# Kernel optimization log

Measured on AMD Instinct MI355X. Metric: run time of the kernel, lower is better.

The kernel has to match this reference:

```python
import jax, jax.numpy as jnp
import numpy as np

B, N_PER, SEQ, DIN, OUT = 16384, 16, 168, 16, 24
H1, H2, OUTF, NH, OLEN, DEG = 128, 128, 64, 4, 128, 4
DH = OUTF // NH
N = B * N_PER
E = N * DEG


def setup_inputs() -> dict:
    key = jax.random.key(0)
    ks = jax.random.split(key, 24)
    rng = np.random.default_rng(0)
    # DEG out-edges per node, destinations confined to the node's own graph block
    src = np.repeat(np.arange(N, dtype=np.int64), DEG)
    dst = (src // N_PER) * N_PER + rng.integers(0, N_PER, size=E).astype(np.int64)
    edge_index = jnp.stack([jnp.asarray(src), jnp.asarray(dst)])
    batch = jnp.asarray(np.arange(N, dtype=np.int64) // N_PER)
    g = lambda i, shape: jax.random.normal(ks[i], shape, jnp.float32) * 0.05
    return dict(
        x=jax.random.normal(ks[0], (N, SEQ), jnp.float32),
        y=jax.random.normal(ks[1], (N, OUT), jnp.float32),
        edge_index=edge_index, batch=batch,
        w1l=g(2, (SEQ, H1)), w1r=g(3, (SEQ, H1)), b1=jnp.zeros((H1,), jnp.float32),
        w2l=g(4, (H1, H2)), w2r=g(5, (H1, H2)), b2=jnp.zeros((H2,), jnp.float32),
        w3l=g(6, (H2, OUTF)), w3r=g(7, (H2, OUTF)), b3=jnp.zeros((OUTF,), jnp.float32),
        tcn_w=g(8, (OUTF, OUTF, 2)), tcn_b=jnp.zeros((OUTF,), jnp.float32),
        wq=g(9, (OUTF, OUTF)), wk=g(10, (OUTF, OUTF)), wv=g(11, (OUTF, OUTF)), wo=g(12, (OUTF, OUTF)),
        wproj=g(13, (OUTF, OLEN)), bproj=jnp.zeros((OLEN,), jnp.float32),
        fc1_w=g(14, (DIN, OLEN, 64)), fc1_b=jnp.zeros((DIN, 64), jnp.float32),
        fc2_w=g(15, (DIN, 64, OUT)), fc2_b=jnp.zeros((DIN, OUT), jnp.float32),
    )


def _sage(h, src, dst, wl, wr, b):
    # PyG SAGEConv: lin_l(mean-aggregated neighbors) + lin_r(self)
    agg = jax.ops.segment_sum(h[src], dst, num_segments=N)
    cnt = jax.ops.segment_sum(jnp.ones((src.shape[0],), h.dtype), dst, num_segments=N)
    agg = agg / jnp.maximum(cnt, 1.0)[:, None]
    return agg @ wl + h @ wr + b


def _forward(x, y, src, dst, w1l, w1r, b1, w2l, w2r, b2, w3l, w3r, b3,
             tcn_w, tcn_b, wq, wk, wv, wo, wproj, bproj, fc1_w, fc1_b, fc2_w, fc2_b):
    h = jax.nn.relu(_sage(x, src, dst, w1l, w1r, b1))
    h = jax.nn.relu(_sage(h, src, dst, w2l, w2r, b2))
    h = _sage(h, src, dst, w3l, w3r, b3)              # [N, 64]
    # ragged->dense batch: batch ids are block-constant with equal counts,
    # so the per-element Python stacking in the original is exactly a reshape
    xb = h.reshape(B, N_PER, OUTF)
    yb = y.reshape(B, N_PER, OUT)
    xt = xb.transpose(0, 2, 1)                        # [B, 64, n]
    # SMTA: causal TCN (kernel 2, channels [64]) with residual, dropout inert
    xp = jnp.pad(xt, ((0, 0), (0, 0), (1, 0)))
    conv = jax.lax.conv_general_dilated(xp, tcn_w, (1,), 'VALID',
                                        dimension_numbers=('NCH', 'OIH', 'NCH'))
    t = jax.nn.relu(conv + tcn_b[None, :, None]) + xt  # [B, 64, n]
    # 4-head self-attention over the node axis
    s = t.transpose(0, 2, 1)                          # [B, n, 64]
    q = (s @ wq).reshape(B, N_PER, NH, DH)
    k = (s @ wk).reshape(B, N_PER, NH, DH)
    v = (s @ wv).reshape(B, N_PER, NH, DH)
    scale = 1.0 / float(np.sqrt(DH))
    att = jax.nn.softmax(jnp.einsum('bqhd,bkhd->bhqk', q, k) * scale, axis=-1)
    o = jnp.einsum('bhqk,bkhd->bqhd', att, v).reshape(B, N_PER, OUTF) @ wo
    feat = o.mean(axis=1) @ wproj + bproj             # [B, 128]
    # per-variable fc heads, vectorized over the DIN heads
    h1 = jax.nn.relu(jnp.einsum('bf,kfh->kbh', feat, fc1_w) + fc1_b[:, None, :])
    pred = jnp.einsum('kbh,kho->kbo', h1, fc2_w) + fc2_b[:, None, :]  # [DIN, B, OUT]
    return pred, yb


def reference(x, y, edge_index, batch, w1l, w1r, b1, w2l, w2r, b2, w3l, w3r, b3,
              tcn_w, tcn_b, wq, wk, wv, wo, wproj, bproj, fc1_w, fc1_b, fc2_w, fc2_b):
    src, dst = edge_index[0], edge_index[1]
    return _forward(x, y, src, dst, w1l, w1r, b1, w2l, w2r, b2, w3l, w3r, b3,
                    tcn_w, tcn_b, wq, wk, wv, wo, wproj, bproj,
                    fc1_w, fc1_b, fc2_w, fc2_b)
```

## Files before the change

kernel.cpp:

```cpp
#include <hip/hip_runtime.h>
#include <cstdint>
#include <cstddef>


typedef __attribute__((ext_vector_type(8))) __bf16 bf16x8;
typedef __attribute__((ext_vector_type(4))) float  f32x4;

#define MFMA16(a,b,c) __builtin_amdgcn_mfma_f32_16x16x32_bf16((a),(b),(c),0,0,0)
#define FENCE() __threadfence_block()

#define NGR    16384
#define EDGES  1048576
#define PRED_ELEMS (16*16384*24)

#define O_W1L 0
#define O_W1R 24576
#define O_W2L 49152
#define O_W2R 65536
#define O_W3L 81920
#define O_W3R 90112
#define O_T0  98304
#define O_T1  102400
#define O_WQ  106496
#define O_WK  110592
#define O_WV  114688
#define O_WO  118784
#define O_FC1 122880
#define O_FC2 253952
#define O_FEAT 286720
#define PREP_TOT 286720

static __device__ __forceinline__ unsigned short f2bf(float f){
  unsigned int u = __builtin_bit_cast(unsigned int, f);
  u += 0x7FFFu + ((u >> 16) & 1u);
  return (unsigned short)(u >> 16);
}
static __device__ __forceinline__ float bf2f(unsigned short h){
  return __builtin_bit_cast(float, (unsigned int)h << 16);
}
static __device__ __forceinline__ bf16x8 ld8(const unsigned short* p){
  return __builtin_bit_cast(bf16x8, *(const uint4*)p);
}
static __device__ __forceinline__ bf16x8 zero8(){
  uint4 u = make_uint4(0u,0u,0u,0u);
  return __builtin_bit_cast(bf16x8, u);
}
static __device__ __forceinline__ unsigned int pkbf2(float a, float b){
  return (unsigned int)f2bf(a) | ((unsigned int)f2bf(b)<<16);
}
static __device__ __forceinline__ bf16x8 u4bf(unsigned int a, unsigned int b,
                                              unsigned int c, unsigned int d){
  uint4 u = make_uint4(a,b,c,d);
  return __builtin_bit_cast(bf16x8, u);
}
static __device__ __forceinline__ bf16x8 shfrag(unsigned int p0, unsigned int p1,
                                                int laneA, int laneB){
  return u4bf((unsigned int)__shfl((int)p0, laneA, 64),
              (unsigned int)__shfl((int)p1, laneA, 64),
              (unsigned int)__shfl((int)p0, laneB, 64),
              (unsigned int)__shfl((int)p1, laneB, 64));
}
static __device__ __forceinline__ bf16x8 xfrag(const float* __restrict__ xrow, int k0){
  int ks = (k0 < 168) ? k0 : 0;
  float4 f0 = *(const float4*)(xrow + ks);
  float4 f1 = *(const float4*)(xrow + ks + 4);
  return u4bf(pkbf2(f0.x,f0.y), pkbf2(f0.z,f0.w),
              pkbf2(f1.x,f1.y), pkbf2(f1.z,f1.w));
}
template<int TOT, int K, int P>
static __device__ __forceinline__ void stageW(const unsigned short* __restrict__ src,
                                              unsigned short* __restrict__ dst, int tid){
  #pragma unroll
  for (int it=0; it<TOT/2048; ++it){
    int idx = it*2048 + tid*8;
    int row = idx / K, col = idx - row*K;
    *(uint4*)(dst + row*P + col) = *(const uint4*)(src + idx);
  }
}

__global__ __launch_bounds__(256) void k_prep(
  const float* __restrict__ w1l, const float* __restrict__ w1r,
  const float* __restrict__ w2l, const float* __restrict__ w2r,
  const float* __restrict__ w3l, const float* __restrict__ w3r,
  const float* __restrict__ tcnw,
  const float* __restrict__ wq, const float* __restrict__ wk,
  const float* __restrict__ wv, const float* __restrict__ wo,
  const float* __restrict__ fc1w, const float* __restrict__ fc2w,
  unsigned short* __restrict__ W)
{
  int idx = blockIdx.x*256 + threadIdx.x;
  if (idx >= PREP_TOT) return;
  float v;
  if      (idx <  24576){ int t=idx;        int n=t/192,k=t%192; v=(k<168)? w1l[k*128+n]:0.f; }
  else if (idx <  49152){ int t=idx- 24576; int n=t/192,k=t%192; v=(k<168)? w1r[k*128+n]:0.f; }
  else if (idx <  65536){ int t=idx- 49152; int n=t/128,k=t%128; v=w2l[k*128+n]; }
  else if (idx <  81920){ int t=idx- 65536; int n=t/128,k=t%128; v=w2r[k*128+n]; }
  else if (idx <  90112){ int t=idx- 81920; int n=t/128,k=t%128; v=w3l[k*64+n]; }
  else if (idx <  98304){ int t=idx- 90112; int n=t/128,k=t%128; v=w3r[k*64+n]; }
  else if (idx < 102400){ int t=idx- 98304; int n=t/64, k=t%64;  v=tcnw[(n*64+k)*2+0]; }
  else if (idx < 106496){ int t=idx-102400; int n=t/64, k=t%64;  v=tcnw[(n*64+k)*2+1]; }
  else if (idx < 110592){ int t=idx-106496; int n=t/64, k=t%64;  v=wq[k*64+n]; }
  else if (idx < 114688){ int t=idx-110592; int n=t/64, k=t%64;  v=wk[k*64+n]; }
  else if (idx < 118784){ int t=idx-114688; int n=t/64, k=t%64;  v=wv[k*64+n]; }
  else if (idx < 122880){ int t=idx-118784; int n=t/64, k=t%64;  v=wo[k*64+n]; }
  else if (idx < 253952){ int t=idx-122880; int kh=t/8192, r=t%8192, n=r/128, k=r%128;
                          v=fc1w[kh*8192 + k*64 + n]; }
  else                  { int t=idx-253952; int kh=t/2048, r=t%2048, n=r/64,  k=r%64;
                          v=(n<24)? fc2w[kh*1536 + k*24 + n] : 0.f; }
  W[idx] = f2bf(v);
}

__global__ __launch_bounds__(256,3) void k_fused(
  const float* __restrict__ x, const int* __restrict__ edst,
  const float* __restrict__ b1, const float* __restrict__ b2,
  const float* __restrict__ b3, const float* __restrict__ tcnb,
  const float* __restrict__ wo, const float* __restrict__ wproj,
  const float* __restrict__ bproj,
  const unsigned short* __restrict__ ws0, unsigned short* __restrict__ feat)
{
  __shared__ alignas(16) unsigned char pool[4*9216];
  __shared__ alignas(16) unsigned short WB[8704];
  const int tid=threadIdx.x, w=tid>>6, lane=tid&63, quad=lane>>4, l15=lane&15;
  unsigned short* AR = (unsigned short*)(pool + w*9216);
  const int gb0 = (blockIdx.x*4 + w)*2;

  unsigned short* Hb = AR;
  unsigned short* X  = AR;
  unsigned short* T  = AR + 2304;
  unsigned short* Qb = AR;
  unsigned short* Pb = AR + 2304;
  float* OMf = (float*)AR;

  const bf16x8 Z = zero8();
  const f32x4  z = {0.f,0.f,0.f,0.f};
  const int laneA = 32*quad + l15, laneB = laneA + 16;

  bf16x8 aA[2];
  #pragma unroll
  for (int g=0; g<2; ++g){
    int dl = edst[(gb0+g)*64 + lane] & 15;
    float c4[4]; float csum = 0.f;
    #pragma unroll
    for (int ss=0; ss<4; ++ss){
      int s = quad*4 + ss; int cc = 0;
      #pragma unroll
      for (int k=0;k<4;++k) cc += (__shfl(dl, s*4+k, 64) == l15) ? 1 : 0;
      c4[ss] = (float)cc; csum += (float)cc;
    }
    csum += __shfl_xor(csum, 16, 64);
    csum += __shfl_xor(csum, 32, 64);
    float ainv = 1.f / fmaxf(csum, 1.f);
    unsigned int p0 = pkbf2(c4[0]*ainv, c4[1]*ainv);
    unsigned int p1 = pkbf2(c4[2]*ainv, c4[3]*ainv);
    bf16x8 t = shfrag(p0, p1, laneA, laneB);
    aA[g] = (quad < 2) ? t : Z;
  }

  const float* xr0 = x + (size_t)(gb0*16 + l15)*168;
  const float* xr1 = xr0 + 16*168;
  bf16x8 xa0[6], xa1[6];
  #pragma unroll
  for (int kc=0;kc<6;++kc){
    xa0[kc] = xfrag(xr0, kc*32 + quad*8);
    xa1[kc] = xfrag(xr1, kc*32 + quad*8);
  }

  #pragma unroll
  for (int cg=0; cg<4; ++cg){
    __syncthreads();
    stageW<6144,192,200>(ws0 + O_W1L + cg*6144, WB, tid);
    __syncthreads();
    f32x4 au[2][2];
    #pragma unroll
    for (int g=0;g<2;++g)
    #pragma unroll
    for (int c=0;c<2;++c) au[g][c]=z;
    #pragma unroll
    for (int kc=0;kc<6;++kc){
      #pragma unroll
      for (int c=0;c<2;++c){
        bf16x8 bl = ld8(WB + (c*16+l15)*200 + kc*32 + quad*8);
        au[0][c] = MFMA16(xa0[kc], bl, au[0][c]);
        au[1][c] = MFMA16(xa1[kc], bl, au[1][c]);
      }
    }
    bf16x8 uf[2][2];
    #pragma unroll
    for (int g=0;g<2;++g)
    #pragma unroll
    for (int c=0;c<2;++c){
      unsigned int p0 = pkbf2(au[g][c][0], au[g][c][1]);
      unsigned int p1 = pkbf2(au[g][c][2], au[g][c][3]);
      uf[g][c] = shfrag(p0,p1,laneA,laneB);
    }
    __syncthreads();
    stageW<6144,192,200>(ws0 + O_W1R + cg*6144, WB, tid);
    __syncthreads();
    f32x4 av_[2][2];
    #pragma unroll
    for (int g=0;g<2;++g)
    #pragma unroll
    for (int c=0;c<2;++c) av_[g][c]=z;
    #pragma unroll
    for (int kc=0;kc<6;++kc){
      #pragma unroll
      for (int c=0;c<2;++c){
        bf16x8 br = ld8(WB + (c*16+l15)*200 + kc*32 + quad*8);
        av_[0][c] = MFMA16(xa0[kc], br, av_[0][c]);
        av_[1][c] = MFMA16(xa1[kc], br, av_[1][c]);
      }
    }
    #pragma unroll
    for (int g=0;g<2;++g)
    #pragma unroll
    for (int c=0;c<2;++c)
      av_[g][c] = MFMA16(aA[g], uf[g][c], av_[g][c]);
    #pragma unroll
    for (int c=0;c<2;++c){
      float bb = b1[cg*32 + c*16 + l15];
      #pragma unroll
      for (int g=0;g<2;++g)
      #pragma unroll
      for (int r=0;r<4;++r)
        Hb[g*2176 + (quad*4+r)*136 + cg*32 + c*16 + l15] = f2bf(fmaxf(av_[g][c][r]+bb, 0.f));
    }
  }
  FENCE();

  {
    ushort4 os[4][2][2];
    #pragma unroll
    for (int cg=0; cg<4; ++cg){
      __syncthreads();
      stageW<4096,128,136>(ws0 + O_W2L + cg*4096, WB, tid);
      __syncthreads();
      bf16x8 uf[2][2];
      {
        f32x4 au[2][2];
        #pragma unroll
        for (int g=0;g<2;++g)
        #pragma unroll
        for (int c=0;c<2;++c) au[g][c]=z;
        #pragma unroll
        for (int kc=0;kc<4;++kc){
          bf16x8 a0 = ld8(Hb +        l15*136 + kc*32 + quad*8);
          bf16x8 a1 = ld8(Hb + 2176 + l15*136 + kc*32 + quad*8);
          #pragma unroll
          for (int c=0;c<2;++c){
            bf16x8 bl = ld8(WB + (c*16+l15)*136 + kc*32 + quad*8);
            au[0][c] = MFMA16(a0, bl, au[0][c]);
            au[1][c] = MFMA16(a1, bl, au[1][c]);
          }
        }
        #pragma unroll
        for (int g=0;g<2;++g)
        #pragma unroll
        for (int c=0;c<2;++c){
          unsigned int p0 = pkbf2(au[g][c][0], au[g][c][1]);
          unsigned int p1 = pkbf2(au[g][c][2], au[g][c][3]);
          uf[g][c] = shfrag(p0,p1,laneA,laneB);
        }
      }
      __syncthreads();
      stageW<4096,128,136>(ws0 + O_W2R + cg*4096, WB, tid);
      __syncthreads();
      {
        f32x4 av_[2][2];
        #pragma unroll
        for (int g=0;g<2;++g)
        #pragma unroll
        for (int c=0;c<2;++c) av_[g][c]=z;
        #pragma unroll
        for (int kc=0;kc<4;++kc){
          bf16x8 a0 = ld8(Hb +        l15*136 + kc*32 + quad*8);
          bf16x8 a1 = ld8(Hb + 2176 + l15*136 + kc*32 + quad*8);
          #pragma unroll
          for (int c=0;c<2;++c){
            bf16x8 br = ld8(WB + (c*16+l15)*136 + kc*32 + quad*8);
            av_[0][c] = MFMA16(a0, br, av_[0][c]);
            av_[1][c] = MFMA16(a1, br, av_[1][c]);
          }
        }
        #pragma unroll
        for (int g=0;g<2;++g)
        #pragma unroll
        for (int c=0;c<2;++c)
          av_[g][c] = MFMA16(aA[g], uf[g][c], av_[g][c]);
        #pragma unroll
        for (int c=0;c<2;++c){
          float bb = b2[cg*32 + c*16 + l15];
          #pragma unroll
          for (int g=0;g<2;++g){
            ushort4 p;
            p.x = f2bf(fmaxf(av_[g][c][0]+bb, 0.f));
            p.y = f2bf(fmaxf(av_[g][c][1]+bb, 0.f));
            p.z = f2bf(fmaxf(av_[g][c][2]+bb, 0.f));
            p.w = f2bf(fmaxf(av_[g][c][3]+bb, 0.f));
            os[cg][g][c] = p;
          }
        }
      }
    }
    #pragma unroll
    for (int cg=0; cg<4; ++cg)
    #pragma unroll
    for (int g=0; g<2; ++g)
    #pragma unroll
    for (int c=0; c<2; ++c){
      unsigned short* bp = Hb + g*2176 + cg*32 + c*16 + l15;
      ushort4 p = os[cg][g][c];
      bp[(quad*4+0)*136] = p.x;
      bp[(quad*4+1)*136] = p.y;
      bp[(quad*4+2)*136] = p.z;
      bp[(quad*4+3)*136] = p.w;
    }
  }
  FENCE();

  {
    bf16x8 uf[2][4];
    __syncthreads();
    stageW<8192,128,136>(ws0 + O_W3L, WB, tid);
    __syncthreads();
    {
      f32x4 au[2][4];
      #pragma unroll
      for (int g=0;g<2;++g)
      #pragma unroll
      for (int c=0;c<4;++c) au[g][c]=z;
      #pragma unroll
      for (int kc=0;kc<4;++kc){
        bf16x8 a0 = ld8(Hb +        l15*136 + kc*32 + quad*8);
        bf16x8 a1 = ld8(Hb + 2176 + l15*136 + kc*32 + quad*8);
        #pragma unroll
        for (int c=0;c<4;++c){
          bf16x8 bl = ld8(WB + (c*16+l15)*136 + kc*32 + quad*8);
          au[0][c] = MFMA16(a0, bl, au[0][c]);
          au[1][c] = MFMA16(a1, bl, au[1][c]);
        }
      }
      #pragma unroll
      for (int g=0;g<2;++g)
      #pragma unroll
      for (int c=0;c<4;++c){
        unsigned int p0 = pkbf2(au[g][c][0], au[g][c][1]);
        unsigned int p1 = pkbf2(au[g][c][2], au[g][c][3]);
        uf[g][c] = shfrag(p0,p1,laneA,laneB);
      }
    }
    __syncthreads();
    stageW<8192,128,136>(ws0 + O_W3R, WB, tid);
    __syncthreads();
    {
      f32x4 av_[2][4];
      #pragma unroll
      for (int g=0;g<2;++g)
      #pragma unroll
      for (int c=0;c<4;++c) av_[g][c]=z;
      #pragma unroll
      for (int kc=0;kc<4;++kc){
        bf16x8 a0 = ld8(Hb +        l15*136 + kc*32 + quad*8);
        bf16x8 a1 = ld8(Hb + 2176 + l15*136 + kc*32 + quad*8);
        #pragma unroll
        for (int c=0;c<4;++c){
          bf16x8 br = ld8(WB + (c*16+l15)*136 + kc*32 + quad*8);
          av_[0][c] = MFMA16(a0, br, av_[0][c]);
          av_[1][c] = MFMA16(a1, br, av_[1][c]);
        }
      }
      #pragma unroll
      for (int g=0;g<2;++g)
      #pragma unroll
      for (int c=0;c<4;++c)
        av_[g][c] = MFMA16(aA[g], uf[g][c], av_[g][c]);
      #pragma unroll
      for (int c=0;c<4;++c){
        float bb = b3[c*16 + l15];
        #pragma unroll
        for (int g=0;g<2;++g)
        #pragma unroll
        for (int r=0;r<4;++r)
          X[g*1152 + (quad*4+r)*72 + c*16 + l15] = f2bf(av_[g][c][r] + bb);
      }
    }
  }
  FENCE();

  {
    f32x4 acct[2][4];
    #pragma unroll
    for (int g=0;g<2;++g)
    #pragma unroll
    for (int c=0;c<4;++c) acct[g][c]=z;
    __syncthreads();
    stageW<4096,64,72>(ws0 + O_T0, WB, tid);
    __syncthreads();
    #pragma unroll
    for (int kc=0;kc<2;++kc){
      bf16x8 as0 = (l15>0) ? ld8(X +        (l15-1)*72 + kc*32 + quad*8) : Z;
      bf16x8 as1 = (l15>0) ? ld8(X + 1152 + (l15-1)*72 + kc*32 + quad*8) : Z;
      #pragma unroll
      for (int c=0;c<4;++c){
        bf16x8 w0 = ld8(WB + (c*16+l15)*72 + kc*32 + quad*8);
        acct[0][c] = MFMA16(as0, w0, acct[0][c]);
        acct[1][c] = MFMA16(as1, w0, acct[1][c]);
      }
    }
    __syncthreads();
    stageW<4096,64,72>(ws0 + O_T1, WB, tid);
    __syncthreads();
    #pragma unroll
    for (int kc=0;kc<2;++kc){
      bf16x8 ax0 = ld8(X +        l15*72 + kc*32 + quad*8);
      bf16x8 ax1 = ld8(X + 1152 + l15*72 + kc*32 + quad*8);
      #pragma unroll
      for (int c=0;c<4;++c){
        bf16x8 w1 = ld8(WB + (c*16+l15)*72 + kc*32 + quad*8);
        acct[0][c] = MFMA16(ax0, w1, acct[0][c]);
        acct[1][c] = MFMA16(ax1, w1, acct[1][c]);
      }
    }
    #pragma unroll
    for (int c=0;c<4;++c){
      float tb = tcnb[c*16 + l15];
      #pragma unroll
      for (int g=0;g<2;++g)
      #pragma unroll
      for (int r=0;r<4;++r){
        float xr = bf2f(X[g*1152 + (quad*4+r)*72 + c*16 + l15]);
        T[g*1152 + (quad*4+r)*72 + c*16 + l15] =
            f2bf(fmaxf(acct[g][c][r]+tb, 0.f) + xr);
      }
    }
  }
  FENCE();

  {
    __syncthreads();
    stageW<4096,64,72>(ws0 + O_WQ, WB, tid);
    __syncthreads();
    f32x4 acc[2][4];
    #pragma unroll
    for (int g=0;g<2;++g)
    #pragma unroll
    for (int c=0;c<4;++c) acc[g][c]=z;
    #pragma unroll
    for (int kc=0;kc<2;++kc){
      bf16x8 t0 = ld8(T +        l15*72 + kc*32 + quad*8);
      bf16x8 t1 = ld8(T + 1152 + l15*72 + kc*32 + quad*8);
      #pragma unroll
      for (int c=0;c<4;++c){
        bf16x8 b = ld8(WB + (c*16+l15)*72 + kc*32 + quad*8);
        acc[0][c] = MFMA16(t0, b, acc[0][c]);
        acc[1][c] = MFMA16(t1, b, acc[1][c]);
      }
    }
    #pragma unroll
    for (int c=0;c<4;++c)
    #pragma unroll
    for (int g=0;g<2;++g)
    #pragma unroll
    for (int r=0;r<4;++r)
      Qb[g*1152 + (quad*4+r)*72 + c*16 + l15] = f2bf(acc[g][c][r]);
  }
  FENCE();

  bf16x8 bK[2][4];
  {
    __syncthreads();
    stageW<4096,64,72>(ws0 + O_WK, WB, tid);
    __syncthreads();
    f32x4 kt[2][4];
    #pragma unroll
    for (int g=0;g<2;++g)
    #pragma unroll
    for (int c=0;c<4;++c) kt[g][c]=z;
    #pragma unroll
    for (int kc=0;kc<2;++kc){
      bf16x8 t0 = ld8(T +        l15*72 + kc*32 + quad*8);
      bf16x8 t1 = ld8(T + 1152 + l15*72 + kc*32 + quad*8);
      #pragma unroll
      for (int c=0;c<4;++c){
        bf16x8 aW = ld8(WB + (c*16+l15)*72 + kc*32 + quad*8);
        kt[0][c] = MFMA16(aW, t0, kt[0][c]);
        kt[1][c] = MFMA16(aW, t1, kt[1][c]);
      }
    }
    #pragma unroll
    for (int g=0;g<2;++g)
    #pragma unroll
    for (int c=0;c<4;++c){
      unsigned int p0 = pkbf2(kt[g][c][0], kt[g][c][1]);
      unsigned int p1 = pkbf2(kt[g][c][2], kt[g][c][3]);
      bf16x8 f = shfrag(p0,p1,laneA,laneB);
      bK[g][c] = (quad < 2) ? f : Z;
    }
  }

  bf16x8 bV[2][4];
  {
    __syncthreads();
    stageW<4096,64,72>(ws0 + O_WV, WB, tid);
    __syncthreads();
    f32x4 acc[2][4];
    #pragma unroll
    for (int g=0;g<2;++g)
    #pragma unroll
    for (int c=0;c<4;++c) acc[g][c]=z;
    #pragma unroll
    for (int kc=0;kc<2;++kc){
      bf16x8 t0 = ld8(T +        l15*72 + kc*32 + quad*8);
      bf16x8 t1 = ld8(T + 1152 + l15*72 + kc*32 + quad*8);
      #pragma unroll
      for (int c=0;c<4;++c){
        bf16x8 b = ld8(WB + (c*16+l15)*72 + kc*32 + quad*8);
        acc[0][c] = MFMA16(t0, b, acc[0][c]);
        acc[1][c] = MFMA16(t1, b, acc[1][c]);
      }
    }
    #pragma unroll
    for (int g=0;g<2;++g)
    #pragma unroll
    for (int c=0;c<4;++c){
      unsigned int p0 = pkbf2(acc[g][c][0], acc[g][c][1]);
      unsigned int p1 = pkbf2(acc[g][c][2], acc[g][c][3]);
      bV[g][c] = shfrag(p0,p1,laneA,laneB);
    }
  }
  FENCE();

  #pragma unroll
  for (int g=0; g<2; ++g){
    unsigned short* Pbg = Pb + g*1024;
    #pragma unroll
    for (int h=0;h<4;++h){
      bf16x8 aQ = (quad < 2) ? ld8(Qb + g*1152 + l15*72 + h*16 + quad*8) : Z;
      f32x4 s4 = MFMA16(aQ, bK[g][h], z);
      #pragma unroll
      for (int r=0;r<4;++r){
        float s = s4[r]*0.25f;
        float m = s;
        m = fmaxf(m, __shfl_xor(m,1,64));
        m = fmaxf(m, __shfl_xor(m,2,64));
        m = fmaxf(m, __shfl_xor(m,4,64));
        m = fmaxf(m, __shfl_xor(m,8,64));
        float p = __expf(s-m);
        float su = p;
        su += __shfl_xor(su,1,64);
        su += __shfl_xor(su,2,64);
        su += __shfl_xor(su,4,64);
        su += __shfl_xor(su,8,64);
        Pbg[(h*16 + quad*4 + r)*16 + l15] = f2bf(p/su);
      }
    }
  }
  FENCE();

  #pragma unroll
  for (int g=0; g<2; ++g){
    unsigned short* Pbg = Pb + g*1024;
    #pragma unroll
    for (int h=0;h<4;++h){
      bf16x8 aP = (quad < 2) ? ld8(Pbg + (h*16 + l15)*16 + quad*8) : Z;
      f32x4 o = MFMA16(aP, bV[g][h], z);
      float cs = o[0]+o[1]+o[2]+o[3];
      cs += __shfl_xor(cs, 16, 64);
      cs += __shfl_xor(cs, 32, 64);
      if (quad == 0) OMf[g*64 + h*16 + l15] = cs * (1.f/16.f);
    }
  }
  FENCE();

  {
    float t0 = 0.f, t1 = 0.f;
    #pragma unroll 8
    for (int d=0; d<64; ++d){
      float wv = wo[d*64 + lane];
      t0 += OMf[d]    * wv;
      t1 += OMf[64+d] * wv;
    }
    OMf[128+lane] = t0;
    OMf[192+lane] = t1;
    FENCE();
    float a00 = bproj[lane], a01 = bproj[lane+64];
    float a10 = a00, a11 = a01;
    #pragma unroll 8
    for (int m=0; m<64; ++m){
      float f0 = OMf[128+m], f1 = OMf[192+m];
      float w0 = wproj[m*128 + lane], w1 = wproj[m*128 + lane + 64];
      a00 += f0*w0; a01 += f0*w1;
      a10 += f1*w0; a11 += f1*w1;
    }
    feat[(size_t)gb0*128 + lane]        = f2bf(a00);
    feat[(size_t)gb0*128 + lane + 64]   = f2bf(a01);
    feat[(size_t)(gb0+1)*128 + lane]      = f2bf(a10);
    feat[(size_t)(gb0+1)*128 + lane + 64] = f2bf(a11);
  }
}

__global__ __launch_bounds__(256,4) void k_heads(
  const unsigned short* __restrict__ ws0,
  const float* __restrict__ fc1b, const float* __restrict__ fc2b,
  float* __restrict__ pred,
  const float4* __restrict__ ysrc, float4* __restrict__ ydst)
{
  __shared__ alignas(16) unsigned short W1s[64*136];
  __shared__ alignas(16) unsigned short W2s[32*72];
  __shared__ alignas(16) unsigned short hh[4*2304];
  const int tid=threadIdx.x, w=tid>>6, lane=tid&63, quad=lane>>4, l15=lane&15;
  const int kh = blockIdx.x >> 7;
  const int rb = (blockIdx.x & 127)*128 + w*32;
  unsigned short* hw = hh + w*2304;
  const unsigned short* featg = ws0 + O_FEAT;
  const unsigned short* W1 = ws0 + O_FC1 + kh*8192;
  const unsigned short* W2 = ws0 + O_FC2 + kh*2048;

  #pragma unroll
  for (int it=0; it<4; ++it){
    int idx = it*2048 + tid*8;
    int row = idx >> 7, col = idx & 127;
    *(uint4*)(W1s + row*136 + col) = *(const uint4*)(W1 + idx);
  }
  {
    int idx = tid*8; int row = idx >> 6, col = idx & 63;
    *(uint4*)(W2s + row*72 + col) = *(const uint4*)(W2 + idx);
  }
  __syncthreads();

  f32x4 z = {0.f,0.f,0.f,0.f};
  f32x4 acc[2][4];
  #pragma unroll
  for (int t=0;t<2;++t)
  #pragma unroll
  for (int c=0;c<4;++c) acc[t][c]=z;
  #pragma unroll
  for (int kc=0;kc<4;++kc){
    bf16x8 a0 = ld8(featg + (size_t)(rb+l15)*128    + kc*32+quad*8);
    bf16x8 a1 = ld8(featg + (size_t)(rb+16+l15)*128 + kc*32+quad*8);
    #pragma unroll
    for (int c=0;c<4;++c){
      bf16x8 b = ld8(W1s + (c*16+l15)*136 + kc*32+quad*8);
      acc[0][c] = MFMA16(a0, b, acc[0][c]);
      acc[1][c] = MFMA16(a1, b, acc[1][c]);
    }
  }
  #pragma unroll
  for (int c=0;c<4;++c){
    float bb = fc1b[kh*64 + c*16+l15];
    #pragma unroll
    for (int t=0;t<2;++t)
    #pragma unroll
    for (int r=0;r<4;++r)
      hw[t*1152 + (quad*4+r)*72 + c*16+l15] = f2bf(fmaxf(acc[t][c][r]+bb, 0.f));
  }
  FENCE();
  f32x4 acc2[2][2];
  #pragma unroll
  for (int t=0;t<2;++t)
  #pragma unroll
  for (int c=0;c<2;++c) acc2[t][c]=z;
  #pragma unroll
  for (int kc=0;kc<2;++kc){
    bf16x8 a0 = ld8(hw +        l15*72 + kc*32+quad*8);
    bf16x8 a1 = ld8(hw + 1152 + l15*72 + kc*32+quad*8);
    #pragma unroll
    for (int c=0;c<2;++c){
      bf16x8 b = ld8(W2s + (c*16+l15)*72 + kc*32+quad*8);
      acc2[0][c] = MFMA16(a0, b, acc2[0][c]);
      acc2[1][c] = MFMA16(a1, b, acc2[1][c]);
    }
  }
  FENCE();
  float* hf = (float*)hw;
  #pragma unroll
  for (int t=0;t<2;++t){
    #pragma unroll
    for (int c=0;c<2;++c){
      int col = c*16+l15;
      if (col < 24){
// ... 59 lines not shown
```

Measured before the change: 475.9 us.

## Double-buffer weight staging with register prefetch across all GEMM phases

Replaces the single shared weight buffer, and its sync-load-sync staging per phase, with two half-size LDS buffers. The next weight chunk is loaded from global memory into registers while MFMAs run on the current buffer, then stored to the other buffer with one barrier. All phases are split into smaller chunks (16 or 32 output columns) so the global-load latency of weights is hidden behind compute. In exchange there are more barriers and phases, extra registers for prefetched data under a 3-block occupancy bound, and smaller MFMA batches per phase.

```diff
diff --git a/kernel.cpp b/kernel.cpp
--- a/kernel.cpp
+++ b/kernel.cpp
@@ -67,16 +67,33 @@
   return u4bf(pkbf2(f0.x,f0.y), pkbf2(f0.z,f0.w),
               pkbf2(f1.x,f1.y), pkbf2(f1.z,f1.w));
 }
-template<int TOT, int K, int P>
-static __device__ __forceinline__ void stageW(const unsigned short* __restrict__ src,
-                                              unsigned short* __restrict__ dst, int tid){
-  #pragma unroll
-  for (int it=0; it<TOT/2048; ++it){
-    int idx = it*2048 + tid*8;
-    int row = idx / K, col = idx - row*K;
-    *(uint4*)(dst + row*P + col) = *(const uint4*)(src + idx);
-  }
-}
+template<int TOT>
+static __device__ __forceinline__ void sload(const unsigned short* __restrict__ src,
+                                             int tid, uint4* r){
+  #pragma unroll
+  for (int i=0;i<TOT/2048;++i)
+    r[i] = *(const uint4*)(src + i*2048 + tid*8);
+  if constexpr ((TOT & 2047) != 0){
+    if (tid < (TOT & 2047)/8)
+      r[TOT/2048] = *(const uint4*)(src + (TOT/2048)*2048 + tid*8);
+  }
+}
+template<int TOT,int K,int P>
+static __device__ __forceinline__ void sstore(unsigned short* __restrict__ dst,
+                                              int tid, const uint4* r){
+  #pragma unroll
+  for (int i=0;i<TOT/2048;++i){
+    int idx = i*2048 + tid*8, row = idx / K;
+    *(uint4*)(dst + row*P + (idx - row*K)) = r[i];
+  }
+  if constexpr ((TOT & 2047) != 0){
+    if (tid < (TOT & 2047)/8){
+      int idx = (TOT/2048)*2048 + tid*8, row = idx / K;
+      *(uint4*)(dst + row*P + (idx - row*K)) = r[TOT/2048];
+    }
+  }
+}
+#define PH_NEXT(TOT,K,P) do{ sstore<TOT,K,P>(WB[cur^1], tid, rg); __syncthreads(); cur^=1; }while(0)
 
 __global__ __launch_bounds__(256) void k_prep(
   const float* __restrict__ w1l, const float* __restrict__ w1r,
@@ -119,7 +136,7 @@
   const unsigned short* __restrict__ ws0, unsigned short* __restrict__ feat)
 {
   __shared__ alignas(16) unsigned char pool[4*9216];
-  __shared__ alignas(16) unsigned short WB[8704];
+  __shared__ alignas(16) unsigned short WB[2][4352];
   const int tid=threadIdx.x, w=tid>>6, lane=tid&63, quad=lane>>4, l15=lane&15;
   unsigned short* AR = (unsigned short*)(pool + w*9216);
   const int gb0 = (blockIdx.x*4 + w)*2;
@@ -135,6 +152,9 @@
   const f32x4  z = {0.f,0.f,0.f,0.f};
   const int laneA = 32*quad + l15, laneB = laneA + 16;
 
+  uint4 rg[2];
+  sload<3072>(ws0 + O_W1L, tid, rg);
+
   bf16x8 aA[2];
   #pragma unroll
   for (int g=0; g<2; ++g){
@@ -150,9 +170,8 @@
     csum += __shfl_xor(csum, 16, 64);
     csum += __shfl_xor(csum, 32, 64);
     float ainv = 1.f / fmaxf(csum, 1.f);
-    unsigned int p0 = pkbf2(c4[0]*ainv, c4[1]*ainv);
-    unsigned int p1 = pkbf2(c4[2]*ainv, c4[3]*ainv);
-    bf16x8 t = shfrag(p0, p1, laneA, laneB);
+    bf16x8 t = shfrag(pkbf2(c4[0]*ainv, c4[1]*ainv),
+                      pkbf2(c4[2]*ainv, c4[3]*ainv), laneA, laneB);
     aA[g] = (quad < 2) ? t : Z;
   }
 
@@ -165,65 +184,45 @@
     xa1[kc] = xfrag(xr1, kc*32 + quad*8);
   }
 
-  #pragma unroll
-  for (int cg=0; cg<4; ++cg){
-    __syncthreads();
-    stageW<6144,192,200>(ws0 + O_W1L + cg*6144, WB, tid);
-    __syncthreads();
-    f32x4 au[2][2];
-    #pragma unroll
-    for (int g=0;g<2;++g)
-    #pragma unroll
-    for (int c=0;c<2;++c) au[g][c]=z;
+  int cur = 0;
+  sstore<3072,192,200>(WB[0], tid, rg);
+  __syncthreads();
+
+  #pragma unroll
+  for (int cg=0; cg<8; ++cg){
+    sload<3072>(ws0 + O_W1R + cg*3072, tid, rg);
+    f32x4 au0=z, au1_=z;
     #pragma unroll
     for (int kc=0;kc<6;++kc){
-      #pragma unroll
-      for (int c=0;c<2;++c){
-        bf16x8 bl = ld8(WB + (c*16+l15)*200 + kc*32 + quad*8);
-        au[0][c] = MFMA16(xa0[kc], bl, au[0][c]);
-        au[1][c] = MFMA16(xa1[kc], bl, au[1][c]);
-      }
-    }
-    bf16x8 uf[2][2];
-    #pragma unroll
-    for (int g=0;g<2;++g)
-    #pragma unroll
-    for (int c=0;c<2;++c){
-      unsigned int p0 = pkbf2(au[g][c][0], au[g][c][1]);
-      unsigned int p1 = pkbf2(au[g][c][2], au[g][c][3]);
-      uf[g][c] = shfrag(p0,p1,laneA,laneB);
-    }
-    __syncthreads();
-    stageW<6144,192,200>(ws0 + O_W1R + cg*6144, WB, tid);
-    __syncthreads();
-    f32x4 av_[2][2];
-    #pragma unroll
-    for (int g=0;g<2;++g)
-    #pragma unroll
-    for (int c=0;c<2;++c) av_[g][c]=z;
+      bf16x8 bl = ld8(WB[cur] + l15*200 + kc*32 + quad*8);
+      au0  = MFMA16(xa0[kc], bl, au0);
+      au1_ = MFMA16(xa1[kc], bl, au1_);
+    }
+    bf16x8 uf0  = shfrag(pkbf2(au0[0],au0[1]),  pkbf2(au0[2],au0[3]),  laneA, laneB);
+    bf16x8 uf1_ = shfrag(pkbf2(au1_[0],au1_[1]), pkbf2(au1_[2],au1_[3]), laneA, laneB);
+    PH_NEXT(3072,192,200);
+
+    if (cg < 7) sload<3072>(ws0 + O_W1L + (cg+1)*3072, tid, rg);
+    else        sload<4096>(ws0 + O_W2L, tid, rg);
+    f32x4 av0=z, av1_=z;
     #pragma unroll
     for (int kc=0;kc<6;++kc){
-      #pragma unroll
-      for (int c=0;c<2;++c){
-        bf16x8 br = ld8(WB + (c*16+l15)*200 + kc*32 + quad*8);
-        av_[0][c] = MFMA16(xa0[kc], br, av_[0][c]);
-        av_[1][c] = MFMA16(xa1[kc], br, av_[1][c]);
-      }
-    }
-    #pragma unroll
-    for (int g=0;g<2;++g)
-    #pragma unroll
-    for (int c=0;c<2;++c)
-      av_[g][c] = MFMA16(aA[g], uf[g][c], av_[g][c]);
-    #pragma unroll
-    for (int c=0;c<2;++c){
-      float bb = b1[cg*32 + c*16 + l15];
-      #pragma unroll
-      for (int g=0;g<2;++g)
-      #pragma unroll
-      for (int r=0;r<4;++r)
-        Hb[g*2176 + (quad*4+r)*136 + cg*32 + c*16 + l15] = f2bf(fmaxf(av_[g][c][r]+bb, 0.f));
-    }
+      bf16x8 br = ld8(WB[cur] + l15*200 + kc*32 + quad*8);
+      av0  = MFMA16(xa0[kc], br, av0);
+      av1_ = MFMA16(xa1[kc], br, av1_);
+    }
+    av0  = MFMA16(aA[0], uf0,  av0);
+    av1_ = MFMA16(aA[1], uf1_, av1_);
+    {
+      float bb = b1[cg*16 + l15];
+      #pragma unroll
+      for (int r=0;r<4;++r){
+        Hb[       (quad*4+r)*136 + cg*16 + l15] = f2bf(fmaxf(av0[r]+bb, 0.f));
+        Hb[2176 + (quad*4+r)*136 + cg*16 + l15] = f2bf(fmaxf(av1_[r]+bb, 0.f));
+      }
+    }
+    if (cg < 7){ PH_NEXT(3072,192,200); }
+    else       { PH_NEXT(4096,128,136); }
   }
   FENCE();
 
@@ -231,23 +230,17 @@
     ushort4 os[4][2][2];
     #pragma unroll
     for (int cg=0; cg<4; ++cg){
-      __syncthreads();
-      stageW<4096,128,136>(ws0 + O_W2L + cg*4096, WB, tid);
-      __syncthreads();
+      sload<4096>(ws0 + O_W2R + cg*4096, tid, rg);
       bf16x8 uf[2][2];
       {
-        f32x4 au[2][2];
-        #pragma unroll
-        for (int g=0;g<2;++g)
-        #pragma unroll
-        for (int c=0;c<2;++c) au[g][c]=z;
+        f32x4 au[2][2] = {{z,z},{z,z}};
         #pragma unroll
         for (int kc=0;kc<4;++kc){
           bf16x8 a0 = ld8(Hb +        l15*136 + kc*32 + quad*8);
           bf16x8 a1 = ld8(Hb + 2176 + l15*136 + kc*32 + quad*8);
           #pragma unroll
           for (int c=0;c<2;++c){
-            bf16x8 bl = ld8(WB + (c*16+l15)*136 + kc*32 + quad*8);
+            bf16x8 bl = ld8(WB[cur] + (c*16+l15)*136 + kc*32 + quad*8);
             au[0][c] = MFMA16(a0, bl, au[0][c]);
             au[1][c] = MFMA16(a1, bl, au[1][c]);
           }
@@ -255,276 +248,391 @@
         #pragma unroll
         for (int g=0;g<2;++g)
         #pragma unroll
-        for (int c=0;c<2;++c){
-          unsigned int p0 = pkbf2(au[g][c][0], au[g][c][1]);
-          unsigned int p1 = pkbf2(au[g][c][2], au[g][c][3]);
-          uf[g][c] = shfrag(p0,p1,laneA,laneB);
-        }
-      }
-      __syncthreads();
-      stageW<4096,128,136>(ws0 + O_W2R + cg*4096, WB, tid);
-      __syncthreads();
+        for (int c=0;c<2;++c)
+          uf[g][c] = shfrag(pkbf2(au[g][c][0],au[g][c][1]),
+                            pkbf2(au[g][c][2],au[g][c][3]), laneA, laneB);
+      }
+      PH_NEXT(4096,128,136);
+
+      if (cg < 3) sload<4096>(ws0 + O_W2L + (cg+1)*4096, tid, rg);
+      else        sload<4096>(ws0 + O_W3L, tid, rg);
       {
-        f32x4 av_[2][2];
-        #pragma unroll
-        for (int g=0;g<2;++g)
-        #pragma unroll
-        for (int c=0;c<2;++c) av_[g][c]=z;
+        f32x4 av[2][2] = {{z,z},{z,z}};
         #pragma unroll
         for (int kc=0;kc<4;++kc){
           bf16x8 a0 = ld8(Hb +        l15*136 + kc*32 + quad*8);
           bf16x8 a1 = ld8(Hb + 2176 + l15*136 + kc*32 + quad*8);
           #pragma unroll
           for (int c=0;c<2;++c){
-            bf16x8 br = ld8(WB + (c*16+l15)*136 + kc*32 + quad*8);
-            av_[0][c] = MFMA16(a0, br, av_[0][c]);
-            av_[1][c] = MFMA16(a1, br, av_[1][c]);
+            bf16x8 br = ld8(WB[cur] + (c*16+l15)*136 + kc*32 + quad*8);
+            av[0][c] = MFMA16(a0, br, av[0][c]);
+            av[1][c] = MFMA16(a1, br, av[1][c]);
           }
         }
         #pragma unroll
         for (int g=0;g<2;++g)
         #pragma unroll
         for (int c=0;c<2;++c)
-          av_[g][c] = MFMA16(aA[g], uf[g][c], av_[g][c]);
+          av[g][c] = MFMA16(aA[g], uf[g][c], av[g][c]);
         #pragma unroll
         for (int c=0;c<2;++c){
           float bb = b2[cg*32 + c*16 + l15];
           #pragma unroll
           for (int g=0;g<2;++g){
             ushort4 p;
-            p.x = f2bf(fmaxf(av_[g][c][0]+bb, 0.f));
-            p.y = f2bf(fmaxf(av_[g][c][1]+bb, 0.f));
-            p.z = f2bf(fmaxf(av_[g][c][2]+bb, 0.f));
-            p.w = f2bf(fmaxf(av_[g][c][3]+bb, 0.f));
+            p.x = f2bf(fmaxf(av[g][c][0]+bb, 0.f));
+            p.y = f2bf(fmaxf(av[g][c][1]+bb, 0.f));
+            p.z = f2bf(fmaxf(av[g][c][2]+bb, 0.f));
+            p.w = f2bf(fmaxf(av[g][c][3]+bb, 0.f));
             os[cg][g][c] = p;
           }
         }
       }
-    }
-    #pragma unroll
-    for (int cg=0; cg<4; ++cg)
-    #pragma unroll
-    for (int g=0; g<2; ++g)
-    #pragma unroll
-    for (int c=0; c<2; ++c){
-      unsigned short* bp = Hb + g*2176 + cg*32 + c*16 + l15;
-      ushort4 p = os[cg][g][c];
-      bp[(quad*4+0)*136] = p.x;
-      bp[(quad*4+1)*136] = p.y;
-      bp[(quad*4+2)*136] = p.z;
-      bp[(quad*4+3)*136] = p.w;
-    }
-  }
-  FENCE();
-
-  {
-    bf16x8 uf[2][4];
-    __syncthreads();
-    stageW<8192,128,136>(ws0 + O_W3L, WB, tid);
-    __syncthreads();
+      if (cg == 3){
+        #pragma unroll
+        for (int c2=0;c2<4;++c2)
+        #pragma unroll
+        for (int g=0;g<2;++g)
+        #pragma unroll
+        for (int c=0;c<2;++c){
+          unsigned short* bp = Hb + g*2176 + c2*32 + c*16 + l15;
+          ushort4 p = os[c2][g][c];
+          bp[(quad*4+0)*136] = p.x;
+          bp[(quad*4+1)*136] = p.y;
+          bp[(quad*4+2)*136] = p.z;
+          bp[(quad*4+3)*136] = p.w;
+        }
+        FENCE();
+      }
+      PH_NEXT(4096,128,136);
+    }
+  }
+
+  bf16x8 uf3[2][4];
+  f32x4  av3[2][4];
+  {
+    sload<4096>(ws0 + O_W3L + 4096, tid, rg);
+    f32x4 au[2][2] = {{z,z},{z,z}};
+    #pragma unroll
+    for (int kc=0;kc<4;++kc){
+      bf16x8 a0 = ld8(Hb +        l15*136 + kc*32 + quad*8);
+      bf16x8 a1 = ld8(Hb + 2176 + l15*136 + kc*32 + quad*8);
+      #pragma unroll
+      for (int c=0;c<2;++c){
+        bf16x8 bl = ld8(WB[cur] + (c*16+l15)*136 + kc*32 + quad*8);
+        au[0][c] = MFMA16(a0, bl, au[0][c]);
+        au[1][c] = MFMA16(a1, bl, au[1][c]);
+      }
+    }
+    #pragma unroll
+    for (int g=0;g<2;++g)
+    #pragma unroll
+    for (int c=0;c<2;++c)
+      uf3[g][c] = shfrag(pkbf2(au[g][c][0],au[g][c][1]),
+                         pkbf2(au[g][c][2],au[g][c][3]), laneA, laneB);
+    PH_NEXT(4096,128,136);
+  }
+  {
+    sload<4096>(ws0 + O_W3R, tid, rg);
+    f32x4 au[2][2] = {{z,z},{z,z}};
+    #pragma unroll
+    for (int kc=0;kc<4;++kc){
+      bf16x8 a0 = ld8(Hb +        l15*136 + kc*32 + quad*8);
+      bf16x8 a1 = ld8(Hb + 2176 + l15*136 + kc*32 + quad*8);
+      #pragma unroll
+      for (int c=0;c<2;++c){
+        bf16x8 bl = ld8(WB[cur] + (c*16+l15)*136 + kc*32 + quad*8);
+        au[0][c] = MFMA16(a0, bl, au[0][c]);
+        au[1][c] = MFMA16(a1, bl, au[1][c]);
+      }
+    }
+    #pragma unroll
+    for (int g=0;g<2;++g)
+    #pragma unroll
+    for (int c=0;c<2;++c)
+      uf3[g][2+c] = shfrag(pkbf2(au[g][c][0],au[g][c][1]),
+                           pkbf2(au[g][c][2],au[g][c][3]), laneA, laneB);
+    PH_NEXT(4096,128,136);
+  }
+  {
+    sload<4096>(ws0 + O_W3R + 4096, tid, rg);
+    #pragma unroll
+    for (int g=0;g<2;++g){ av3[g][0]=z; av3[g][1]=z; }
+    #pragma unroll
+    for (int kc=0;kc<4;++kc){
+      bf16x8 a0 = ld8(Hb +        l15*136 + kc*32 + quad*8);
+      bf16x8 a1 = ld8(Hb + 2176 + l15*136 + kc*32 + quad*8);
+      #pragma unroll
+      for (int c=0;c<2;++c){
+        bf16x8 br = ld8(WB[cur] + (c*16+l15)*136 + kc*32 + quad*8);
+        av3[0][c] = MFMA16(a0, br, av3[0][c]);
+        av3[1][c] = MFMA16(a1, br, av3[1][c]);
+      }
+    }
+    #pragma unroll
+    for (int g=0;g<2;++g)
+    #pragma unroll
+    for (int c=0;c<2;++c)
+      av3[g][c] = MFMA16(aA[g], uf3[g][c], av3[g][c]);
+    PH_NEXT(4096,128,136);
+  }
+  {
+    sload<2048>(ws0 + O_T0, tid, rg);
+    #pragma unroll
+    for (int g=0;g<2;++g){ av3[g][2]=z; av3[g][3]=z; }
+    #pragma unroll
+    for (int kc=0;kc<4;++kc){
+      bf16x8 a0 = ld8(Hb +        l15*136 + kc*32 + quad*8);
+      bf16x8 a1 = ld8(Hb + 2176 + l15*136 + kc*32 + quad*8);
+      #pragma unroll
+      for (int c=0;c<2;++c){
+        bf16x8 br = ld8(WB[cur] + (c*16+l15)*136 + kc*32 + quad*8);
+        av3[0][2+c] = MFMA16(a0, br, av3[0][2+c]);
+        av3[1][2+c] = MFMA16(a1, br, av3[1][2+c]);
+      }
+    }
+    #pragma unroll
+    for (int g=0;g<2;++g)
+    #pragma unroll
+    for (int c=0;c<2;++c)
+      av3[g][2+c] = MFMA16(aA[g], uf3[g][2+c], av3[g][2+c]);
+    #pragma unroll
+    for (int c=0;c<4;++c){
+      float bb = b3[c*16 + l15];
+      #pragma unroll
+      for (int g=0;g<2;++g)
+      #pragma unroll
+      for (int r=0;r<4;++r)
+        X[g*1152 + (quad*4+r)*72 + c*16 + l15] = f2bf(av3[g][c][r] + bb);
+    }
+    FENCE();
+    PH_NEXT(2048,64,72);
+  }
+
+  {
+    f32x4 acct[2][2] = {{z,z},{z,z}};
     {
-      f32x4 au[2][4];
-      #pragma unroll
-      for (int g=0;g<2;++g)
-      #pragma unroll
-      for (int c=0;c<4;++c) au[g][c]=z;
-      #pragma unroll
-      for (int kc=0;kc<4;++kc){
-        bf16x8 a0 = ld8(Hb +        l15*136 + kc*32 + quad*8);
-        bf16x8 a1 = ld8(Hb + 2176 + l15*136 + kc*32 + quad*8);
-        #pragma unroll
-        for (int c=0;c<4;++c){
-          bf16x8 bl = ld8(WB + (c*16+l15)*136 + kc*32 + quad*8);
-          au[0][c] = MFMA16(a0, bl, au[0][c]);
-          au[1][c] = MFMA16(a1, bl, au[1][c]);
-        }
-      }
-      #pragma unroll
-      for (int g=0;g<2;++g)
-      #pragma unroll
-      for (int c=0;c<4;++c){
-        unsigned int p0 = pkbf2(au[g][c][0], au[g][c][1]);
-        unsigned int p1 = pkbf2(au[g][c][2], au[g][c][3]);
-        uf[g][c] = shfrag(p0,p1,laneA,laneB);
-      }
-    }
-    __syncthreads();
-    stageW<8192,128,136>(ws0 + O_W3R, WB, tid);
-    __syncthreads();
+      sload<2048>(ws0 + O_T1, tid, rg);
+      #pragma unroll
+      for (int kc=0;kc<2;++kc){
+        bf16x8 as0 = (l15>0) ? ld8(X +        (l15-1)*72 + kc*32 + quad*8) : Z;
+        bf16x8 as1 = (l15>0) ? ld8(X + 1152 + (l15-1)*72 + kc*32 + quad*8) : Z;
+        #pragma unroll
+        for (int c=0;c<2;++c){
+          bf16x8 w0 = ld8(WB[cur] + (c*16+l15)*72 + kc*32 + quad*8);
+          acct[0][c] = MFMA16(as0, w0, acct[0][c]);
+          acct[1][c] = MFMA16(as1, w0, acct[1][c]);
+        }
+      }
+      PH_NEXT(2048,64,72);
+    }
     {
-      f32x4 av_[2][4];
-      #pragma unroll
-      for (int g=0;g<2;++g)
-      #pragma unroll
-      for (int c=0;c<4;++c) av_[g][c]=z;
-      #pragma unroll
-      for (int kc=0;kc<4;++kc){
-        bf16x8 a0 = ld8(Hb +        l15*136 + kc*32 + quad*8);
-        bf16x8 a1 = ld8(Hb + 2176 + l15*136 + kc*32 + quad*8);
-        #pragma unroll
-        for (int c=0;c<4;++c){
-          bf16x8 br = ld8(WB + (c*16+l15)*136 + kc*32 + quad*8);
-          av_[0][c] = MFMA16(a0, br, av_[0][c]);
-          av_[1][c] = MFMA16(a1, br, av_[1][c]);
-        }
-      }
-      #pragma unroll
-      for (int g=0;g<2;++g)
-      #pragma unroll
-      for (int c=0;c<4;++c)
-        av_[g][c] = MFMA16(aA[g], uf[g][c], av_[g][c]);
-      #pragma unroll
-      for (int c=0;c<4;++c){
-        float bb = b3[c*16 + l15];
+      sload<2048>(ws0 + O_T0 + 2048, tid, rg);
+      #pragma unroll
+      for (int kc=0;kc<2;++kc){
+        bf16x8 ax0 = ld8(X +        l15*72 + kc*32 + quad*8);
+        bf16x8 ax1 = ld8(X + 1152 + l15*72 + kc*32 + quad*8);
+        #pragma unroll
+        for (int c=0;c<2;++c){
+          bf16x8 w1 = ld8(WB[cur] + (c*16+l15)*72 + kc*32 + quad*8);
+          acct[0][c] = MFMA16(ax0, w1, acct[0][c]);
+          acct[1][c] = MFMA16(ax1, w1, acct[1][c]);
+        }
+      }
+      #pragma unroll
+      for (int c=0;c<2;++c){
+        int col = c*16 + l15;
+        float tb = tcnb[col];
         #pragma unroll
         for (int g=0;g<2;++g)
         #pragma unroll
-        for (int r=0;r<4;++r)
-          X[g*1152 + (quad*4+r)*72 + c*16 + l15] = f2bf(av_[g][c][r] + bb);
-      }
-    }
-  }
-  FENCE();
-
-  {
-    f32x4 acct[2][4];
-    #pragma unroll
-    for (int g=0;g<2;++g)
-    #pragma unroll
-    for (int c=0;c<4;++c) acct[g][c]=z;
-    __syncthreads();
-    stageW<4096,64,72>(ws0 + O_T0, WB, tid);
-    __syncthreads();
-    #pragma unroll
-    for (int kc=0;kc<2;++kc){
-      bf16x8 as0 = (l15>0) ? ld8(X +        (l15-1)*72 + kc*32 + quad*8) : Z;
-      bf16x8 as1 = (l15>0) ? ld8(X + 1152 + (l15-1)*72 + kc*32 + quad*8) : Z;
-      #pragma unroll
-      for (int c=0;c<4;++c){
-        bf16x8 w0 = ld8(WB + (c*16+l15)*72 + kc*32 + quad*8);
-        acct[0][c] = MFMA16(as0, w0, acct[0][c]);
-        acct[1][c] = MFMA16(as1, w0, acct[1][c]);
-      }
-    }
-    __syncthreads();
-    stageW<4096,64,72>(ws0 + O_T1, WB, tid);
-    __syncthreads();
-    #pragma unroll
-    for (int kc=0;kc<2;++kc){
-      bf16x8 ax0 = ld8(X +        l15*72 + kc*32 + quad*8);
-      bf16x8 ax1 = ld8(X + 1152 + l15*72 + kc*32 + quad*8);
-      #pragma unroll
-      for (int c=0;c<4;++c){
-        bf16x8 w1 = ld8(WB + (c*16+l15)*72 + kc*32 + quad*8);
-        acct[0][c] = MFMA16(ax0, w1, acct[0][c]);
-        acct[1][c] = MFMA16(ax1, w1, acct[1][c]);
-      }
-    }
-    #pragma unroll
-    for (int c=0;c<4;++c){
-      float tb = tcnb[c*16 + l15];
-      #pragma unroll
-      for (int g=0;g<2;++g)
-      #pragma unroll
-      for (int r=0;r<4;++r){
-        float xr = bf2f(X[g*1152 + (quad*4+r)*72 + c*16 + l15]);
-        T[g*1152 + (quad*4+r)*72 + c*16 + l15] =
-            f2bf(fmaxf(acct[g][c][r]+tb, 0.f) + xr);
-      }
-    }
-  }
-  FENCE();
-
-  {
-    __syncthreads();
-    stageW<4096,64,72>(ws0 + O_WQ, WB, tid);
-    __syncthreads();
-    f32x4 acc[2][4];
-    #pragma unroll
-    for (int g=0;g<2;++g)
-    #pragma unroll
-    for (int c=0;c<4;++c) acc[g][c]=z;
+        for (int r=0;r<4;++r){
+          float xr = bf2f(X[g*1152 + (quad*4+r)*72 + col]);
+          T[g*1152 + (quad*4+r)*72 + col] = f2bf(fmaxf(acct[g][c][r]+tb, 0.f) + xr);
+        }
+      }
+      PH_NEXT(2048,64,72);
+    }
+    f32x4 acc2[2][2] = {{z,z},{z,z}};
+    {
+      sload<2048>(ws0 + O_T1 + 2048, tid, rg);
+      #pragma unroll
+      for (int kc=0;kc<2;++kc){
+        bf16x8 as0 = (l15>0) ? ld8(X +        (l15-1)*72 + kc*32 + quad*8) : Z;
+        bf16x8 as1 = (l15>0) ? ld8(X + 1152 + (l15-1)*72 + kc*32 + quad*8) : Z;
+        #pragma unroll
+        for (int c=0;c<2;++c){
+          bf16x8 w0 = ld8(WB[cur] + (c*16+l15)*72 + kc*32 + quad*8);
+          acc2[0][c] = MFMA16(as0, w0, acc2[0][c]);
+          acc2[1][c] = MFMA16(as1, w0, acc2[1][c]);
+        }
+      }
+      PH_NEXT(2048,64,72);
+    }
+    {
+      sload<2048>(ws0 + O_WQ, tid, rg);
+      #pragma unroll
+      for (int kc=0;kc<2;++kc){
+        bf16x8 ax0 = ld8(X +        l15*72 + kc*32 + quad*8);
+        bf16x8 ax1 = ld8(X + 1152 + l15*72 + kc*32 + quad*8);
+        #pragma unroll
+        for (int c=0;c<2;++c){
+          bf16x8 w1 = ld8(WB[cur] + (c*16+l15)*72 + kc*32 + quad*8);
+          acc2[0][c] = MFMA16(ax0, w1, acc2[0][c]);
+          acc2[1][c] = MFMA16(ax1, w1, acc2[1][c]);
+        }
+      }
+      #pragma unroll
+      for (int c=0;c<2;++c){
+        int col = 32 + c*16 + l15;
+        float tb = tcnb[col];
+        #pragma unroll
+        for (int g=0;g<2;++g)
+        #pragma unroll
+        for (int r=0;r<4;++r){
+          float xr = bf2f(X[g*1152 + (quad*4+r)*72 + col]);
+          T[g*1152 + (quad*4+r)*72 + col] = f2bf(fmaxf(acc2[g][c][r]+tb, 0.f) + xr);
+        }
+      }
+      FENCE();
+      PH_NEXT(2048,64,72);
+    }
+  }
+
+  {
+    sload<2048>(ws0 + O_WQ + 2048, tid, rg);
+    f32x4 aq[2][2] = {{z,z},{z,z}};
     #pragma unroll
     for (int kc=0;kc<2;++kc){
       bf16x8 t0 = ld8(T +        l15*72 + kc*32 + quad*8);
       bf16x8 t1 = ld8(T + 1152 + l15*72 + kc*32 + quad*8);
       #pragma unroll
-      for (int c=0;c<4;++c){
-        bf16x8 b = ld8(WB + (c*16+l15)*72 + kc*32 + quad*8);
-        acc[0][c] = MFMA16(t0, b, acc[0][c]);
-        acc[1][c] = MFMA16(t1, b, acc[1][c]);
-      }
-    }
-    #pragma unroll
-    for (int c=0;c<4;++c)
+      for (int c=0;c<2;++c){
+        bf16x8 b = ld8(WB[cur] + (c*16+l15)*72 + kc*32 + quad*8);
+        aq[0][c] = MFMA16(t0, b, aq[0][c]);
+        aq[1][c] = MFMA16(t1, b, aq[1][c]);
+      }
+    }
+    #pragma unroll
+    for (int c=0;c<2;++c)
     #pragma unroll
     for (int g=0;g<2;++g)
     #pragma unroll
     for (int r=0;r<4;++r)
-      Qb[g*1152 + (quad*4+r)*72 + c*16 + l15] = f2bf(acc[g][c][r]);
-  }
-  FENCE();
-
-  bf16x8 bK[2][4];
-  {
-    __syncthreads();
-    stageW<4096,64,72>(ws0 + O_WK, WB, tid);
-    __syncthreads();
-    f32x4 kt[2][4];
-    #pragma unroll
-    for (int g=0;g<2;++g)
-    #pragma unroll
-    for (int c=0;c<4;++c) kt[g][c]=z;
+      Qb[g*1152 + (quad*4+r)*72 + c*16 + l15] = f2bf(aq[g][c][r]);
+    PH_NEXT(2048,64,72);
+  }
+  {
+    sload<2048>(ws0 + O_WK, tid, rg);
+    f32x4 aq[2][2] = {{z,z},{z,z}};
     #pragma unroll
     for (int kc=0;kc<2;++kc){
       bf16x8 t0 = ld8(T +        l15*72 + kc*32 + quad*8);
       bf16x8 t1 = ld8(T + 1152 + l15*72 + kc*32 + quad*8);
       #pragma unroll
+      for (int c=0;c<2;++c){
+        bf16x8 b = ld8(WB[cur] + (c*16+l15)*72 + kc*32 + quad*8);
+        aq[0][c] = MFMA16(t0, b, aq[0][c]);
+        aq[1][c] = MFMA16(t1, b, aq[1][c]);
+      }
+    }
+    #pragma unroll
+    for (int c=0;c<2;++c)
+    #pragma unroll
+    for (int g=0;g<2;++g)
+    #pragma unroll
+    for (int r=0;r<4;++r)
+      Qb[g*1152 + (quad*4+r)*72 + 32 + c*16 + l15] = f2bf(aq[g][c][r]);
+    PH_NEXT(2048,64,72);
+  }
+
+  bf16x8 bK[2][4];
+  {
+    f32x4 kt[2][4];
+    {
+      sload<2048>(ws0 + O_WK + 2048, tid, rg);
+      #pragma unroll
+      for (int g=0;g<2;++g){ kt[g][0]=z; kt[g][1]=z; }
+      #pragma unroll
+      for (int kc=0;kc<2;++kc){
+        bf16x8 t0 = ld8(T +        l15*72 + kc*32 + quad*8);
+        bf16x8 t1 = ld8(T + 1152 + l15*72 + kc*32 + quad*8);
+        #pragma unroll
+        for (int c=0;c<2;++c){
+          bf16x8 aW = ld8(WB[cur] + (c*16+l15)*72 + kc*32 + quad*8);
+          kt[0][c] = MFMA16(aW, t0, kt[0][c]);
+          kt[1][c] = MFMA16(aW, t1, kt[1][c]);
+        }
+      }
+      PH_NEXT(2048,64,72);
+    }
+    {
+      sload<2048>(ws0 + O_WV, tid, rg);
+      #pragma unroll
+      for (int g=0;g<2;++g){ kt[g][2]=z; kt[g][3]=z; }
+      #pragma unroll
+      for (int kc=0;kc<2;++kc){
+        bf16x8 t0 = ld8(T +        l15*72 + kc*32 + quad*8);
+        bf16x8 t1 = ld8(T + 1152 + l15*72 + kc*32 + quad*8);
+        #pragma unroll
+        for (int c=0;c<2;++c){
+          bf16x8 aW = ld8(WB[cur] + (c*16+l15)*72 + kc*32 + quad*8);
+          kt[0][2+c] = MFMA16(aW, t0, kt[0][2+c]);
+          kt[1][2+c] = MFMA16(aW, t1, kt[1][2+c]);
+        }
+      }
+      #pragma unroll
+      for (int g=0;g<2;++g)
+      #pragma unroll
       for (int c=0;c<4;++c){
-        bf16x8 aW = ld8(WB + (c*16+l15)*72 + kc*32 + quad*8);
-        kt[0][c] = MFMA16(aW, t0, kt[0][c]);
-        kt[1][c] = MFMA16(aW, t1, kt[1][c]);
-      }
-    }
-    #pragma unroll
-    for (int g=0;g<2;++g)
-    #pragma unroll
-    for (int c=0;c<4;++c){
-      unsigned int p0 = pkbf2(kt[g][c][0], kt[g][c][1]);
-      unsigned int p1 = pkbf2(kt[g][c][2], kt[g][c][3]);
-      bf16x8 f = shfrag(p0,p1,laneA,laneB);
-      bK[g][c] = (quad < 2) ? f : Z;
+        bf16x8 f = shfrag(pkbf2(kt[g][c][0],kt[g][c][1]),
+                          pkbf2(kt[g][c][2],kt[g][c][3]), laneA, laneB);
+        bK[g][c] = (quad < 2) ? f : Z;
+      }
+      PH_NEXT(2048,64,72);
     }
   }
 
   bf16x8 bV[2][4];
   {
-    __syncthreads();
-    stageW<4096,64,72>(ws0 + O_WV, WB, tid);
-    __syncthreads();
-    f32x4 acc[2][4];
-    #pragma unroll
-    for (int g=0;g<2;++g)
-    #pragma unroll
-    for (int c=0;c<4;++c) acc[g][c]=z;
-    #pragma unroll
-    for (int kc=0;kc<2;++kc){
-      bf16x8 t0 = ld8(T +        l15*72 + kc*32 + quad*8);
-      bf16x8 t1 = ld8(T + 1152 + l15*72 + kc*32 + quad*8);
-      #pragma unroll
-      for (int c=0;c<4;++c){
-        bf16x8 b = ld8(WB + (c*16+l15)*72 + kc*32 + quad*8);
-        acc[0][c] = MFMA16(t0, b, acc[0][c]);
-        acc[1][c] = MFMA16(t1, b, acc[1][c]);
-      }
-    }
-    #pragma unroll
-    for (int g=0;g<2;++g)
-    #pragma unroll
-    for (int c=0;c<4;++c){
-      unsigned int p0 = pkbf2(acc[g][c][0], acc[g][c][1]);
-      unsigned int p1 = pkbf2(acc[g][c][2], acc[g][c][3]);
-      bV[g][c] = shfrag(p0,p1,laneA,laneB);
+    f32x4 vv[2][4];
+    {
+      sload<2048>(ws0 + O_WV + 2048, tid, rg);
+      #pragma unroll
+      for (int g=0;g<2;++g){ vv[g][0]=z; vv[g][1]=z; }
+      #pragma unroll
+      for (int kc=0;kc<2;++kc){
+        bf16x8 t0 = ld8(T +        l15*72 + kc*32 + quad*8);
+        bf16x8 t1 = ld8(T + 1152 + l15*72 + kc*32 + quad*8);
+        #pragma unroll
+        for (int c=0;c<2;++c){
+          bf16x8 b = ld8(WB[cur] + (c*16+l15)*72 + kc*32 + quad*8);
+          vv[0][c] = MFMA16(t0, b, vv[0][c]);
+          vv[1][c] = MFMA16(t1, b, vv[1][c]);
+        }
+      }
+      PH_NEXT(2048,64,72);
+    }
+    {
+      #pragma unroll
+      for (int g=0;g<2;++g){ vv[g][2]=z; vv[g][3]=z; }
+      #pragma unroll
+      for (int kc=0;kc<2;++kc){
+        bf16x8 t0 = ld8(T +        l15*72 + kc*32 + quad*8);
+        bf16x8 t1 = ld8(T + 1152 + l15*72 + kc*32 + quad*8);
+        #pragma unroll
+        for (int c=0;c<2;++c){
+          bf16x8 b = ld8(WB[cur] + (c*16+l15)*72 + kc*32 + quad*8);
+          vv[0][2+c] = MFMA16(t0, b, vv[0][2+c]);
+          vv[1][2+c] = MFMA16(t1, b, vv[1][2+c]);
+        }
+      }
+      #pragma unroll
+      for (int g=0;g<2;++g)
+      #pragma unroll
+      for (int c=0;c<4;++c)
+        bV[g][c] = shfrag(pkbf2(vv[g][c][0],vv[g][c][1]),
+                          pkbf2(vv[g][c][2],vv[g][c][3]), laneA, laneB);
     }
   }
   FENCE();
```

Result: slower. 516.1 us (+8.4%).
